# Kernel tuning notes

Measured on AMD Instinct MI355X. Metric: run time of the kernel, lower is better.

## Reference

```python
import jax, jax.numpy as jnp
import numpy as np

V, E, H = 32000, 512, 1024  # vocab, embedding_dim, hidden_dim
B, T = 16, 256


def _lstm_layer(x, mask, Wx, Wh, b):
    """Keras-semantics masked LSTM. x:[B,T,D], mask:[B,T] bool.
    Gate order i,f,g,o (Keras). Masked steps carry h,c (and output) forward."""
    Bx, Tx, _ = x.shape
    Hh = Wh.shape[0]
    xs = jnp.swapaxes(x, 0, 1)                       # [T,B,D]
    ms = jnp.swapaxes(mask, 0, 1)[..., None]         # [T,B,1]
    # hoist the input projection out of the scan (one big GEMM)
    xz = jnp.einsum('tbd,dh->tbh', xs, Wx) + b       # [T,B,4H]

    def step(carry, inp):
        h, c = carry
        zx, mt = inp
        z = zx + h @ Wh
        i, f, g, o = jnp.split(z, 4, axis=-1)
        i = jax.nn.sigmoid(i)
        f = jax.nn.sigmoid(f)
        g = jnp.tanh(g)
        o = jax.nn.sigmoid(o)
        c_new = f * c + i * g
        h_new = o * jnp.tanh(c_new)
        h2 = jnp.where(mt, h_new, h)
        c2 = jnp.where(mt, c_new, c)
        return (h2, c2), h2

    init = (jnp.zeros((Bx, Hh), x.dtype), jnp.zeros((Bx, Hh), x.dtype))
    _, ys = jax.lax.scan(step, init, (xz, ms))
    return jnp.swapaxes(ys, 0, 1)                    # [B,T,H]


def setup_inputs() -> dict:
    key = jax.random.key(0)
    ks = jax.random.split(key, 10)
    s = 0.02
    tokens = jax.random.randint(ks[0], (B, T), 0, V)
    emb = jax.random.normal(ks[1], (V, E), jnp.float32) * s
    Wx0 = jax.random.normal(ks[2], (E, 4 * H), jnp.float32) * s
    Wh0 = jax.random.normal(ks[3], (H, 4 * H), jnp.float32) * s
    b0 = jnp.zeros((4 * H,), jnp.float32).at[H:2 * H].set(1.0)  # unit_forget_bias
    Wx1 = jax.random.normal(ks[4], (H, 4 * H), jnp.float32) * s
    Wh1 = jax.random.normal(ks[5], (H, 4 * H), jnp.float32) * s
    b1 = jnp.zeros((4 * H,), jnp.float32).at[H:2 * H].set(1.0)
    Wout = jax.random.normal(ks[6], (H, V), jnp.float32) * s
    bout = jnp.zeros((V,), jnp.float32)
    return {"tokens": tokens, "emb": emb, "Wx0": Wx0, "Wh0": Wh0, "b0": b0,
            "Wx1": Wx1, "Wh1": Wh1, "b1": b1, "Wout": Wout, "bout": bout}


def reference(tokens, emb, Wx0, Wh0, b0, Wx1, Wh1, b1, Wout, bout):
    mask = tokens != 0                               # mask_zero=True
    x = emb[tokens]                                  # [B,T,E]
    x = _lstm_layer(x, mask, Wx0, Wh0, b0)
    x = _lstm_layer(x, mask, Wx1, Wh1, b1)
    logits = x @ Wout + bout                         # [B,T,V]
    fm = mask[..., None].astype(logits.dtype)
    onehot0 = jnp.zeros((V,), logits.dtype).at[0].set(1.0)  # tf.eye(V)[0]
    return logits * fm + onehot0 * (1.0 - fm)
```

## Files before the change

kernel.cpp:

```cpp
#include <hip/hip_runtime.h>

#define B_ 16
#define T_ 256
#define E_ 512
#define H_ 1024
#define V_ 32000
#define HX16 (H_ * 16)
#define SENT 0xFFFFFFFFu

typedef float f32x4 __attribute__((ext_vector_type(4)));
typedef short short8 __attribute__((ext_vector_type(8)));

typedef __attribute__((address_space(1))) const void gas_t;
typedef __attribute__((address_space(3))) void las_t;

__device__ __forceinline__ unsigned short f2bf(float x) {
    unsigned int u = __float_as_uint(x);
    u += 0x7FFF + ((u >> 16) & 1);
    return (unsigned short)(u >> 16);
}
__device__ __forceinline__ float bf2f(unsigned short b) {
    return __uint_as_float(((unsigned int)b) << 16);
}
__device__ __forceinline__ float fsig(float x) {
    return __fdividef(1.f, 1.f + __expf(-x));
}
__device__ __forceinline__ float ftanh(float x) {
    float xc = fminf(fmaxf(x, -15.f), 15.f);
    float e  = __expf(-2.f * xc);
    return __fdividef(1.f - e, 1.f + e);
}

__global__ __launch_bounds__(256)
void gather_cvt_k(const int* __restrict__ tokens, const float* __restrict__ emb,
                  unsigned short* __restrict__ Ah, unsigned short* __restrict__ Al)
{
    int i  = blockIdx.x * 256 + threadIdx.x;
    int bt = i >> 7;
    int e4 = i & 127;
    float4 v = ((const float4*)(emb + (size_t)tokens[bt] * E_))[e4];
    ushort4 h, l;
    h.x = f2bf(v.x); l.x = f2bf(v.x - bf2f(h.x));
    h.y = f2bf(v.y); l.y = f2bf(v.y - bf2f(h.y));
    h.z = f2bf(v.z); l.z = f2bf(v.z - bf2f(h.z));
    h.w = f2bf(v.w); l.w = f2bf(v.w - bf2f(h.w));
    ((ushort4*)Ah)[i] = h;
    ((ushort4*)Al)[i] = l;
}

__global__ __launch_bounds__(256)
void twz_k(const float* __restrict__ W, unsigned short* __restrict__ Bh,
           unsigned short* __restrict__ Bl, int Kd, int Nfull, int n0)
{
    __shared__ float tile[32][33];
    int t  = threadIdx.x;
    int tx = t & 31, ty = t >> 5;
    int nb = blockIdx.x * 32, kb = blockIdx.y * 32;
    #pragma unroll
    for (int i = 0; i < 4; ++i)
        tile[ty + i * 8][tx] = W[(size_t)(kb + ty + i * 8) * Nfull + n0 + nb + tx];
    __syncthreads();
    #pragma unroll
    for (int i = 0; i < 4; ++i) {
        float v = tile[tx][ty + i * 8];
        unsigned short h = f2bf(v), l = f2bf(v - bf2f(h));
        size_t o = (size_t)(nb + ty + i * 8) * Kd + kb + tx;
        Bh[o] = h; Bl[o] = l;
    }
}

template<int DO_MASK>
__global__ __launch_bounds__(256)
void mgemm_k(const unsigned short* __restrict__ Ah, const unsigned short* __restrict__ Al,
             const unsigned short* __restrict__ Bh, const unsigned short* __restrict__ Bl,
             const float* __restrict__ bias, float* __restrict__ C,
             const int* __restrict__ tokens, int K, int ldc, int n0)
{
    __shared__ unsigned short LDSS[4][128 * 64];

    const int tid  = threadIdx.x;
    const int nwg = gridDim.x * gridDim.y;
    int lin = blockIdx.y * gridDim.x + blockIdx.x;
    lin = (lin & 7) * (nwg >> 3) + (lin >> 3);
    const int bm   = (lin / gridDim.x) * 128;
    const int bn   = (lin % gridDim.x) * 128;
    const int w    = tid >> 6, lane = tid & 63;
    const int wm   = (w >> 1) * 64, wn = (w & 1) * 64;
    const int l15  = lane & 15, lhi = lane >> 4;

    const unsigned short* gp = (w == 0) ? Ah : (w == 1) ? Al : (w == 2) ? Bh : Bl;
    const int rb = (w < 2) ? bm : bn;
    const int srow = lane >> 3;
    const int scol = (lane & 7) ^ srow;
    unsigned short* lbase = &LDSS[w][0];

    f32x4 acc[4][4];
    #pragma unroll
    for (int mi = 0; mi < 4; ++mi)
        #pragma unroll
        for (int ni = 0; ni < 4; ++ni) {
            f32x4 z = {0.f, 0.f, 0.f, 0.f};
            acc[mi][ni] = z;
        }

    for (int kt = 0; kt < K; kt += 64) {
        #pragma unroll
        for (int c = 0; c < 16; ++c) {
            const unsigned short* src =
                gp + (size_t)(rb + c * 8 + srow) * K + kt + scol * 8;
            __builtin_amdgcn_global_load_lds((gas_t*)src,
                                             (las_t*)(lbase + c * 512), 16, 0, 0);
        }
        __syncthreads();
        #pragma unroll
        for (int ks = 0; ks < 2; ++ks) {
            short8 ah[4], al[4], bh[4], bl[4];
            const int s = ks * 4 + lhi;
            #pragma unroll
            for (int mi = 0; mi < 4; ++mi) {
                int m = wm + mi * 16 + l15;
                int off = m * 64 + ((s ^ (m & 7)) * 8);
                ah[mi] = *(const short8*)(&LDSS[0][off]);
                al[mi] = *(const short8*)(&LDSS[1][off]);
            }
            #pragma unroll
            for (int ni = 0; ni < 4; ++ni) {
                int n = wn + ni * 16 + l15;
                int off = n * 64 + ((s ^ (n & 7)) * 8);
                bh[ni] = *(const short8*)(&LDSS[2][off]);
                bl[ni] = *(const short8*)(&LDSS[3][off]);
            }
            #pragma unroll
            for (int mi = 0; mi < 4; ++mi)
                #pragma unroll
                for (int ni = 0; ni < 4; ++ni) {
                    acc[mi][ni] = __builtin_amdgcn_mfma_f32_16x16x32_bf16(
                        ah[mi], bh[ni], acc[mi][ni], 0, 0, 0);
                    acc[mi][ni] = __builtin_amdgcn_mfma_f32_16x16x32_bf16(
                        ah[mi], bl[ni], acc[mi][ni], 0, 0, 0);
                    acc[mi][ni] = __builtin_amdgcn_mfma_f32_16x16x32_bf16(
                        al[mi], bh[ni], acc[mi][ni], 0, 0, 0);
                }
        }
        __syncthreads();
    }

    #pragma unroll
    for (int mi = 0; mi < 4; ++mi) {
        #pragma unroll
        for (int r = 0; r < 4; ++r) {
            int row = bm + wm + mi * 16 + lhi * 4 + r;
            bool msk = true;
            if (DO_MASK) msk = (tokens[row] != 0);
            #pragma unroll
            for (int ni = 0; ni < 4; ++ni) {
                int col = bn + wn + ni * 16 + l15;
                float v = acc[mi][ni][r] + bias[n0 + col];
                if (DO_MASK && !msk) v = ((n0 + col) == 0) ? 1.f : 0.f;
                C[(size_t)row * ldc + n0 + col] = v;
            }
        }
    }
}

__global__ __launch_bounds__(256)
void wprep_k(const float* __restrict__ Wh, uint4* __restrict__ WhF)
{
    int flat = blockIdx.x * 256 + threadIdx.x;
    int l  = flat & 63;
    int kf = (flat >> 6) & 3;
    int ct = (flat >> 8) & 3;
    int w  = (flat >> 10) & 7;
    int bx = flat >> 13;
    int k0  = w * 128 + kf * 32 + 8 * (l >> 4);
    int col = ct * H_ + bx * 16 + (l & 15);
    unsigned short hi[8], lo[8];
    #pragma unroll
    for (int j = 0; j < 8; ++j) {
        float v = Wh[(size_t)(k0 + j) * (4 * H_) + col];
        hi[j] = f2bf(v); lo[j] = f2bf(v - bf2f(hi[j]));
    }
    size_t base = ((((size_t)bx * 8 + w) * 4 + ct) * 4 + kf) * 2;
    WhF[(base + 0) * 64 + l] = *(uint4*)hi;
    WhF[(base + 1) * 64 + l] = *(uint4*)lo;
}

__global__ __launch_bounds__(256)
void sfill_k(uint4* __restrict__ p, unsigned n4)
{
    uint4 s = {SENT, SENT, SENT, SENT};
    for (size_t i = (size_t)blockIdx.x * 256 + threadIdx.x; i < n4;
         i += (size_t)gridDim.x * 256)
        p[i] = s;
}

#define MFMA_FROM_HD()                                                        \
    do {                                                                      \
        f32x4 a0 = {0.f,0.f,0.f,0.f}, a1 = a0, a2 = a0, a3 = a0;              \
        _Pragma("unroll")                                                     \
        for (int kf = 0; kf < 4; ++kf) {                                      \
            unsigned short hh[8], hl[8];                                      \
            _Pragma("unroll")                                                 \
            for (int j = 0; j < 8; ++j) {                                     \
                unsigned d = hd[kf][j];                                       \
                hh[j] = (unsigned short)(d >> 16);                            \
                hl[j] = (unsigned short)(d & 0xFFFFu);                        \
            }                                                                 \
            short8 ah = *(short8*)hh, al = *(short8*)hl;                      \
            a0 = __builtin_amdgcn_mfma_f32_16x16x32_bf16(ah, Bhi[0][kf], a0, 0,0,0); \
            a0 = __builtin_amdgcn_mfma_f32_16x16x32_bf16(ah, Blo[0][kf], a0, 0,0,0); \
            a0 = __builtin_amdgcn_mfma_f32_16x16x32_bf16(al, Bhi[0][kf], a0, 0,0,0); \
            a1 = __builtin_amdgcn_mfma_f32_16x16x32_bf16(ah, Bhi[1][kf], a1, 0,0,0); \
            a1 = __builtin_amdgcn_mfma_f32_16x16x32_bf16(ah, Blo[1][kf], a1, 0,0,0); \
            a1 = __builtin_amdgcn_mfma_f32_16x16x32_bf16(al, Bhi[1][kf], a1, 0,0,0); \
            a2 = __builtin_amdgcn_mfma_f32_16x16x32_bf16(ah, Bhi[2][kf], a2, 0,0,0); \
            a2 = __builtin_amdgcn_mfma_f32_16x16x32_bf16(ah, Blo[2][kf], a2, 0,0,0); \
            a2 = __builtin_amdgcn_mfma_f32_16x16x32_bf16(al, Bhi[2][kf], a2, 0,0,0); \
            a3 = __builtin_amdgcn_mfma_f32_16x16x32_bf16(ah, Bhi[3][kf], a3, 0,0,0); \
            a3 = __builtin_amdgcn_mfma_f32_16x16x32_bf16(ah, Blo[3][kf], a3, 0,0,0); \
            a3 = __builtin_amdgcn_mfma_f32_16x16x32_bf16(al, Bhi[3][kf], a3, 0,0,0); \
        }                                                                     \
        _Pragma("unroll")                                                     \
        for (int r = 0; r < 4; ++r) {                                         \
            Rs2[r * 2048 + (0 * 8 + w) * 64 + l] = a0[r];                     \
            Rs2[r * 2048 + (1 * 8 + w) * 64 + l] = a1[r];                     \
            Rs2[r * 2048 + (2 * 8 + w) * 64 + l] = a2[r];                     \
            Rs2[r * 2048 + (3 * 8 + w) * 64 + l] = a3[r];                     \
        }                                                                     \
    } while (0)

#define ISSUE_H(HT_BASE, TIDX)                                                \
    do {                                                                      \
        const unsigned* hTp_ = (HT_BASE) + (size_t)(TIDX) * HX16;             \
        _Pragma("unroll")                                                     \
        for (int kf = 0; kf < 4; ++kf) {                                      \
            const int k0 = w * 128 + kf * 32 + 8 * lhi;                       \
            _Pragma("unroll")                                                 \
            for (int j = 0; j < 8; ++j) {                                     \
                const unsigned* ap = hTp_ + (k0 + j) * 16 + l15;              \
                asm volatile("global_load_dword %0, %1, off sc0 sc1"          \
                             : "=&v"(hd[kf][j]) : "v"(ap));                   \
            }                                                                 \
        }                                                                     \
    } while (0)

#define HD_BAD(BADV)                                                          \
    do {                                                                      \
        _Pragma("unroll")                                                     \
        for (int kf = 0; kf < 4; ++kf)                                        \
            _Pragma("unroll")                                                 \
            for (int j = 0; j < 8; ++j)                                       \
                (BADV) |= (hd[kf][j] == SENT);                                \
    } while (0)

__global__ __launch_bounds__(512, 1)
void lstm_fused_k(const float* __restrict__ xz0,
                  const uint4* __restrict__ WhF0,
                  const uint4* __restrict__ WxF1,
                  const uint4* __restrict__ WhF1,
                  const float* __restrict__ b1v,
                  float* __restrict__ xz1,
                  unsigned* __restrict__ hT0,
                  unsigned* __restrict__ hT1,
                  unsigned short* __restrict__ Ahp,
                  unsigned short* __restrict__ Alp,
                  const int* __restrict__ tokens)
{
    __shared__ float Rs2[4 * 2048];

    const int tid  = threadIdx.x;
    const int role = blockIdx.x >> 6;
    const int bx   = blockIdx.x & 63;
    const int w    = tid >> 6;
    const int l    = tid & 63;
    const int l15  = l & 15, lhi = l >> 4;
    const int u    = bx * 16 + l15;
    const int bl   = lhi * 4 + w;
    const size_t bt_base = (size_t)bl * T_;

    short8 Bhi[4][4], Blo[4][4];
    {
        const uint4* wimg = (role == 0) ? WhF0 : (role == 1) ? WxF1 : WhF1;
        const uint4* p = wimg + (((size_t)bx * 8 + w) * 32) * 64;
        #pragma unroll
        for (int ct = 0; ct < 4; ++ct)
            #pragma unroll
            for (int kf = 0; kf < 4; ++kf) {
                uint4 hv = p[((ct * 4 + kf) * 2 + 0) * 64 + l];
                uint4 lv = p[((ct * 4 + kf) * 2 + 1) * 64 + l];
                Bhi[ct][kf] = *(short8*)&hv;
                Blo[ct][kf] = *(short8*)&lv;
            }
    }
    #pragma unroll
    for (int ct = 0; ct < 4; ++ct)
        #pragma unroll
        for (int kf = 0; kf < 4; ++kf) {
            asm volatile("" : "+v"(Bhi[ct][kf]));
            asm volatile("" : "+v"(Blo[ct][kf]));
        }

    if (role == 0) {
        float c1 = 0.f, h1v = 0.f;
        for (int t = 0; t < T_; ++t) {
            float xzr[4];
            int tok = 0;
            if (w < 4) {
                size_t bt = bt_base + t;
                #pragma unroll
                for (int ct = 0; ct < 4; ++ct)
                    xzr[ct] = xz0[bt * 4096 + (size_t)ct * H_ + u];
                tok = tokens[bt];
            }
            if (t > 0) {
                unsigned hd[4][8];
                while (true) {
                    ISSUE_H(hT0, t - 1);
                    asm volatile("s_waitcnt vmcnt(0)" ::: "memory");
                    __builtin_amdgcn_sched_barrier(0);
                    bool bad = false;
                    HD_BAD(bad);
                    if (!__any(bad)) break;
                    __builtin_amdgcn_s_sleep(2);
                }
                MFMA_FROM_HD();
            }
            __syncthreads();

            if (w < 4) {
                float z[4];
                #pragma unroll
                for (int ct = 0; ct < 4; ++ct) {
                    float s = 0.f;
                    if (t > 0) {
                        #pragma unroll
                        for (int w2 = 0; w2 < 8; ++w2)
                            s += Rs2[w * 2048 + (ct * 8 + w2) * 64 + l];
                    }
                    z[ct] = s + xzr[ct];
                }
                float i_ = fsig(z[0]);
                float f_ = fsig(z[1]);
                float g_ = ftanh(z[2]);
                float o_ = fsig(z[3]);
                float c_new = f_ * c1 + i_ * g_;
                float h_new = o_ * ftanh(c_new);
                bool  m  = (tok != 0);
                float h2 = m ? h_new : h1v;
                c1  = m ? c_new : c1;
                h1v = h2;
                unsigned short hh = f2bf(h2);
                unsigned short hl = f2bf(h2 - bf2f(hh));
                unsigned pack = ((unsigned)hh << 16) | hl;
                __hip_atomic_store(&hT0[(size_t)t * HX16 + u * 16 + bl], pack,
                                   __ATOMIC_RELAXED, __HIP_MEMORY_SCOPE_AGENT);
            }
            __syncthreads();
        }
    } else if (role == 1) {
        float b1r[4];
        if (w < 4) {
            #pragma unroll
            for (int ct = 0; ct < 4; ++ct) b1r[ct] = b1v[ct * H_ + u];
        }
        for (int t = 0; t < T_; ++t) {
            {
                unsigned hd[4][8];
                while (true) {
                    ISSUE_H(hT0, t);
                    asm volatile("s_waitcnt vmcnt(0)" ::: "memory");
                    __builtin_amdgcn_sched_barrier(0);
                    bool bad = false;
                    HD_BAD(bad);
                    if (!__any(bad)) break;
                    __builtin_amdgcn_s_sleep(2);
                }
                MFMA_FROM_HD();
            }
            __syncthreads();

            if (w < 4) {
                size_t bt = bt_base + t;
                #pragma unroll
                for (int ct = 0; ct < 4; ++ct) {
                    float s = 0.f;
                    #pragma unroll
                    for (int w2 = 0; w2 < 8; ++w2)
                        s += Rs2[w * 2048 + (ct * 8 + w2) * 64 + l];
                    float z = s + b1r[ct];
                    const float* ap = xz1 + bt * 4096 + (size_t)ct * H_ + u;
                    asm volatile("global_store_dword %0, %1, off sc0 sc1"
                                 :: "v"(ap), "v"(z) : "memory");
                }
            }
            __syncthreads();
        }
    } else {
        float c1 = 0.f, h1v = 0.f;
        for (int t = 0; t < T_; ++t) {
            unsigned hd[4][8];
            unsigned xzu[4];
            int tok = 0;
            size_t bt = bt_base + t;
            if (w < 4) tok = tokens[bt];
            while (true) {
                if (w < 4) {
                    #pragma unroll
                    for (int ct = 0; ct < 4; ++ct) {
                        const float* ap = xz1 + bt * 4096 + (size_t)ct * H_ + u;
                        asm volatile("global_load_dword %0, %1, off sc0 sc1"
                                     : "=&v"(xzu[ct]) : "v"(ap));
                    }
                }
                if (t > 0) ISSUE_H(hT1, t - 1);
                asm volatile("s_waitcnt vmcnt(0)" ::: "memory");
                __builtin_amdgcn_sched_barrier(0);
                bool bad = false;
                if (w < 4) {
                    #pragma unroll
                    for (int ct = 0; ct < 4; ++ct) bad |= (xzu[ct] == SENT);
                }
                if (t > 0) HD_BAD(bad);
                if (!__any(bad)) break;
                __builtin_amdgcn_s_sleep(2);
            }
            if (t > 0) MFMA_FROM_HD();
            __syncthreads();

            if (w < 4) {
                float z[4];
                #pragma unroll
                for (int ct = 0; ct < 4; ++ct) {
                    float s = 0.f;
                    if (t > 0) {
                        #pragma unroll
                        for (int w2 = 0; w2 < 8; ++w2)
                            s += Rs2[w * 2048 + (ct * 8 + w2) * 64 + l];
                    }
                    z[ct] = s + __uint_as_float(xzu[ct]);
                }
                float i_ = fsig(z[0]);
                float f_ = fsig(z[1]);
                float g_ = ftanh(z[2]);
                float o_ = fsig(z[3]);
                float c_new = f_ * c1 + i_ * g_;
                float h_new = o_ * ftanh(c_new);
                bool  m  = (tok != 0);
                float h2 = m ? h_new : h1v;
                c1  = m ? c_new : c1;
                h1v = h2;
                unsigned short hh = f2bf(h2);
                unsigned short hl = f2bf(h2 - bf2f(hh));
                unsigned pack = ((unsigned)hh << 16) | hl;
                __hip_atomic_store(&hT1[(size_t)t * HX16 + u * 16 + bl], pack,
                                   __ATOMIC_RELAXED, __HIP_MEMORY_SCOPE_AGENT);
                Ahp[bt * (size_t)H_ + u] = hh;
                Alp[bt * (size_t)H_ + u] = hl;
            }
            __syncthreads();
        }
    }
}

extern "C" void kernel_launch(void* const* d_in, const int* in_sizes, int n_in,
                              void* d_out, int out_size, void* d_ws, size_t ws_size,
                              hipStream_t stream)
{
    const int*   tokens = (const int*)d_in[0];
    const float* emb    = (const float*)d_in[1];
    const float* Wx0    = (const float*)d_in[2];
    const float* Wh0    = (const float*)d_in[3];
    const float* b0     = (const float*)d_in[4];
    const float* Wx1    = (const float*)d_in[5];
    const float* Wh1    = (const float*)d_in[6];
    const float* b1     = (const float*)d_in[7];
    const float* Wout   = (const float*)d_in[8];
    const float* bout   = (const float*)d_in[9];
    float* out = (float*)d_out;

    unsigned short* wsu = (unsigned short*)d_ws;
    const size_t BPL = (size_t)16000 * 1024;
    const size_t AP  = (size_t)4096 * 1024;
    unsigned short* Bh  = wsu;
    unsigned short* Bl  = wsu + BPL;
    unsigned short* Ahp = wsu + 2 * BPL;
    unsigned short* Alp = Ahp + AP;

    float* f    = (float*)d_out;
    float* xz0  = f;
    float* WhF0 = xz0 + (size_t)4096 * 4096;
    float* WxF1 = WhF0 + (size_t)1024 * 4096;
    float* WhF1 = WxF1 + (size_t)1024 * 4096;
    float* xz1  = WhF1 + (size_t)1024 * 4096;
    unsigned* hT0 = (unsigned*)(xz1 + (size_t)4096 * 4096);
    unsigned* hT1 = hT0 + (size_t)T_ * HX16;

    dim3 blk(256);

    gather_cvt_k<<<2048, blk, 0, stream>>>(tokens, emb, Ahp, Alp);
    twz_k<<<dim3(128, 16), blk, 0, stream>>>(Wx0, Bh, Bl, 512, 4096, 0);
    mgemm_k<0><<<dim3(32, 32), blk, 0, stream>>>(Ahp, Alp, Bh, Bl, b0, xz0,
                                                 nullptr, 512, 4096, 0);
    wprep_k<<<2048, blk, 0, stream>>>(Wh0, (uint4*)WhF0);
    wprep_k<<<2048, blk, 0, stream>>>(Wx1, (uint4*)WxF1);
    wprep_k<<<2048, blk, 0, stream>>>(Wh1, (uint4*)WhF1);
    sfill_k<<<4096, blk, 0, stream>>>((uint4*)xz1, 6291456u);
    {
        void* args[] = {(void*)&xz0, (void*)&WhF0, (void*)&WxF1, (void*)&WhF1,
                        (void*)&b1, (void*)&xz1, (void*)&hT0, (void*)&hT1,
                        (void*)&Ahp, (void*)&Alp, (void*)&tokens};
        hipLaunchCooperativeKernel((void*)lstm_fused_k, dim3(192), dim3(512),
                                   args, 0, stream);
    }
    twz_k<<<dim3(500, 32), blk, 0, stream>>>(Wout, Bh, Bl, 1024, 32000, 0);
    mgemm_k<1><<<dim3(125, 32), blk, 0, stream>>>(Ahp, Alp, Bh, Bl, bout, out,
                                                  tokens, 1024, 32000, 0);
    twz_k<<<dim3(500, 32), blk, 0, stream>>>(Wout, Bh, Bl, 1024, 32000, 16000);
    mgemm_k<1><<<dim3(125, 32), blk, 0, stream>>>(Ahp, Alp, Bh, Bl, bout, out,
                                                  tokens, 1024, 32000, 16000);
}
```

Baseline: 2.339 ms.

## Overlap Wout bf16 split conversion with LSTM recurrence via extra cooperative blocks

Adds a fourth role of 64 blocks to the cooperative LSTM kernel. These blocks transpose the first half of Wout and split it into bf16 hi/lo parts while the latency-bound recurrence runs on the other blocks, which removes one standalone twz_k launch from the critical path. The three wprep launches are also merged into a single kernel launch. The cost is a larger cooperative grid and extra memory traffic competing with the recurrence's polling and loads.

```diff
diff --git a/kernel.cpp b/kernel.cpp
--- a/kernel.cpp
+++ b/kernel.cpp
@@ -164,9 +164,14 @@
 }
 
 __global__ __launch_bounds__(256)
-void wprep_k(const float* __restrict__ Wh, uint4* __restrict__ WhF)
-{
-    int flat = blockIdx.x * 256 + threadIdx.x;
+void wprep3_k(const float* __restrict__ W0, const float* __restrict__ W1,
+              const float* __restrict__ W2, uint4* __restrict__ F0,
+              uint4* __restrict__ F1, uint4* __restrict__ F2)
+{
+    int sel = blockIdx.x >> 11;
+    const float* Wh = (sel == 0) ? W0 : (sel == 1) ? W1 : W2;
+    uint4* WhF = (sel == 0) ? F0 : (sel == 1) ? F1 : F2;
+    int flat = (blockIdx.x & 2047) * 256 + threadIdx.x;
     int l  = flat & 63;
     int kf = (flat >> 6) & 3;
     int ct = (flat >> 8) & 3;
@@ -264,7 +269,10 @@
                   unsigned* __restrict__ hT1,
                   unsigned short* __restrict__ Ahp,
                   unsigned short* __restrict__ Alp,
-                  const int* __restrict__ tokens)
+                  const int* __restrict__ tokens,
+                  const float* __restrict__ Wout,
+                  unsigned short* __restrict__ BhW,
+                  unsigned short* __restrict__ BlW)
 {
     __shared__ float Rs2[4 * 2048];
 
@@ -279,7 +287,7 @@
     const size_t bt_base = (size_t)bl * T_;
 
     short8 Bhi[4][4], Blo[4][4];
-    {
+    if (role < 3) {
         const uint4* wimg = (role == 0) ? WhF0 : (role == 1) ? WxF1 : WhF1;
         const uint4* p = wimg + (((size_t)bx * 8 + w) * 32) * 64;
         #pragma unroll
@@ -291,14 +299,14 @@
                 Bhi[ct][kf] = *(short8*)&hv;
                 Blo[ct][kf] = *(short8*)&lv;
             }
-    }
-    #pragma unroll
-    for (int ct = 0; ct < 4; ++ct)
         #pragma unroll
-        for (int kf = 0; kf < 4; ++kf) {
-            asm volatile("" : "+v"(Bhi[ct][kf]));
-            asm volatile("" : "+v"(Blo[ct][kf]));
-        }
+        for (int ct = 0; ct < 4; ++ct)
+            #pragma unroll
+            for (int kf = 0; kf < 4; ++kf) {
+                asm volatile("" : "+v"(Bhi[ct][kf]));
+                asm volatile("" : "+v"(Blo[ct][kf]));
+            }
+    }
 
     if (role == 0) {
         float c1 = 0.f, h1v = 0.f;
@@ -395,7 +403,7 @@
             }
             __syncthreads();
         }
-    } else {
+    } else if (role == 2) {
         float c1 = 0.f, h1v = 0.f;
         for (int t = 0; t < T_; ++t) {
             unsigned hd[4][8];
@@ -459,6 +467,28 @@
             }
             __syncthreads();
         }
+    } else {
+        float* tile = Rs2 + (tid >> 8) * 1056;
+        const int tsub = tid & 255;
+        const int tx = tsub & 31, ty = tsub >> 5;
+        for (int it = 0; it < 125; ++it) {
+            int tl = bx * 250 + it * 2 + (tid >> 8);
+            int nb = (tl % 500) * 32;
+            int kb = (tl / 500) * 32;
+            #pragma unroll
+            for (int i = 0; i < 4; ++i)
+                tile[(ty + i * 8) * 33 + tx] =
+                    Wout[(size_t)(kb + ty + i * 8) * (size_t)V_ + nb + tx];
+            __syncthreads();
+            #pragma unroll
+            for (int i = 0; i < 4; ++i) {
+                float v = tile[tx * 33 + ty + i * 8];
+                unsigned short h2 = f2bf(v), l2 = f2bf(v - bf2f(h2));
+                size_t o = (size_t)(nb + ty + i * 8) * H_ + kb + tx;
+                BhW[o] = h2; BlW[o] = l2;
+            }
+            __syncthreads();
+        }
     }
 }
 
@@ -501,18 +531,17 @@
     twz_k<<<dim3(128, 16), blk, 0, stream>>>(Wx0, Bh, Bl, 512, 4096, 0);
     mgemm_k<0><<<dim3(32, 32), blk, 0, stream>>>(Ahp, Alp, Bh, Bl, b0, xz0,
                                                  nullptr, 512, 4096, 0);
-    wprep_k<<<2048, blk, 0, stream>>>(Wh0, (uint4*)WhF0);
-    wprep_k<<<2048, blk, 0, stream>>>(Wx1, (uint4*)WxF1);
-    wprep_k<<<2048, blk, 0, stream>>>(Wh1, (uint4*)WhF1);
+    wprep3_k<<<6144, blk, 0, stream>>>(Wh0, Wx1, Wh1, (uint4*)WhF0,
+                                       (uint4*)WxF1, (uint4*)WhF1);
     sfill_k<<<4096, blk, 0, stream>>>((uint4*)xz1, 6291456u);
     {
         void* args[] = {(void*)&xz0, (void*)&WhF0, (void*)&WxF1, (void*)&WhF1,
                         (void*)&b1, (void*)&xz1, (void*)&hT0, (void*)&hT1,
-                        (void*)&Ahp, (void*)&Alp, (void*)&tokens};
-        hipLaunchCooperativeKernel((void*)lstm_fused_k, dim3(192), dim3(512),
+                        (void*)&Ahp, (void*)&Alp, (void*)&tokens,
+                        (void*)&Wout, (void*)&Bh, (void*)&Bl};
+        hipLaunchCooperativeKernel((void*)lstm_fused_k, dim3(256), dim3(512),
                                    args, 0, stream);
     }
-    twz_k<<<dim3(500, 32), blk, 0, stream>>>(Wout, Bh, Bl, 1024, 32000, 0);
     mgemm_k<1><<<dim3(125, 32), blk, 0, stream>>>(Ahp, Alp, Bh, Bl, bout, out,
                                                   tokens, 1024, 32000, 0);
     twz_k<<<dim3(500, 32), blk, 0, stream>>>(Wout, Bh, Bl, 1024, 32000, 16000);
```

Result: no change. 2.343 ms (+0.2%).
